# Performance work log

Hardware: AMD Instinct MI355X
Metric: run time of the kernel (lower is better)

Reference implementation:

```python
import jax, jax.numpy as jnp
import numpy as np

NEG_INF = jnp.float32(-1e30)


def setup_inputs() -> dict:
    key = jax.random.key(0)
    k1, k2, k3, k4 = jax.random.split(key, 4)
    B, L1, L2, H = 64, 1024, 1024, 128
    x = jax.random.normal(k1, (B, L1, H), dtype=jnp.float32)
    y = jax.random.normal(k2, (B, L2, H), dtype=jnp.float32)
    y_mask = jax.random.uniform(k3, (B, L2)) < 0.2
    W = jax.random.normal(k4, (H, H), dtype=jnp.float32) * (1.0 / np.sqrt(H))
    b = jnp.zeros((H,), dtype=jnp.float32)
    return {"x": x, "y": y, "y_mask": y_mask, "W": W, "b": b}


def reference(x, y, y_mask, W, b):
    # shared linear + relu projections (torch Linear: x @ W.T + b)
    x_proj = jax.nn.relu(jnp.einsum("bld,hd->blh", x, W) + b)  # [B, L1, H]
    y_proj = jax.nn.relu(jnp.einsum("bld,hd->blh", y, W) + b)  # [B, L2, H]
    # unscaled cross-attention scores
    scores = jnp.einsum("bih,bjh->bij", x_proj, y_proj)  # [B, L1, L2]
    scores = jnp.where(y_mask[:, None, :], NEG_INF, scores)
    alpha = jax.nn.softmax(scores, axis=-1)  # [B, L1, L2]
    # weighted sum over original (unprojected) y
    matched_seq = jnp.einsum("bij,bjh->bih", alpha, y)  # [B, L1, H]
    return matched_seq
```

## Files before the change

kernel.cpp:

```cpp
#include <hip/hip_runtime.h>
#include <hip/hip_bf16.h>


typedef __attribute__((ext_vector_type(8))) short    s8v;
typedef __attribute__((ext_vector_type(8))) _Float16 h8v;
typedef __attribute__((ext_vector_type(4))) _Float16 h4v;
typedef __attribute__((ext_vector_type(4))) float    f4v;

#define BDIM 256

__device__ __forceinline__ f4v mfma_bf16(s8v a, s8v b, f4v c) {
    return __builtin_amdgcn_mfma_f32_16x16x32_bf16(a, b, c, 0, 0, 0);
}
__device__ __forceinline__ f4v mfma_f16(h8v a, h8v b, f4v c) {
    return __builtin_amdgcn_mfma_f32_16x16x32_f16(a, b, c, 0, 0, 0);
}
__device__ __forceinline__ void tsplit(float v, short& hi, short& lo) {
    unsigned b = __builtin_bit_cast(unsigned, v);
    unsigned hb = b & 0xFFFF0000u;
    float res = v - __builtin_bit_cast(float, hb);
    hi = (short)(hb >> 16);
    lo = (short)(__builtin_bit_cast(unsigned, res) >> 16);
}

typedef const __attribute__((address_space(1))) unsigned int gu32;
typedef __attribute__((address_space(3))) unsigned int lu32;
__device__ __forceinline__ void gld_lds16(const void* g, void* l) {
    __builtin_amdgcn_global_load_lds((gu32*)g, (lu32*)l, 16, 0, 0);
}

__global__ __launch_bounds__(1024) void prep_kernel(
    const unsigned int* __restrict__ mraw, unsigned int* __restrict__ orw,
    const float* __restrict__ W, short* __restrict__ Whsw, short* __restrict__ Wlsw)
{
    if (blockIdx.x == 1) {
        for (int idx = threadIdx.x; idx < 16384; idx += 1024) {
            int r = idx >> 7, c = idx & 127;
            short hi, lo; tsplit(W[idx], hi, lo);
            int cs = (((c >> 3) ^ (r & 15)) << 3) | (c & 7);
            Whsw[r * 128 + cs] = hi;
            Wlsw[r * 128 + cs] = lo;
        }
        return;
    }
    __shared__ unsigned int sOrAll, sOrOdd;
    if (threadIdx.x == 0) { sOrAll = 0u; sOrOdd = 0u; }
    __syncthreads();
    unsigned int oa = 0u, oo = 0u;
    for (int i = threadIdx.x; i < 16384; i += 1024) {
        unsigned int v = mraw[i];
        oa |= v;
        if (i & 1) oo |= v;
    }
    atomicOr(&sOrAll, oa);
    atomicOr(&sOrOdd, oo);
    __syncthreads();
    if (threadIdx.x == 0) { orw[0] = sOrAll; orw[1] = sOrOdd; }
}

__global__ __launch_bounds__(BDIM, 4) void proj_kernel(
    const float* __restrict__ X, const float* __restrict__ Y,
    const short* __restrict__ Whsw, const short* __restrict__ Wlsw,
    const float* __restrict__ bias, const unsigned int* __restrict__ orw,
    const unsigned int* __restrict__ mraw, unsigned char* __restrict__ nm,
    _Float16* __restrict__ XPf, _Float16* __restrict__ YPsw,
    _Float16* __restrict__ YTsw)
{
    __shared__ short sW[2][64][128];

    const int gid = blockIdx.x;
    const float* src; int local;
    const bool isY = (gid >= 1024);
    if (!isY) { src = X; local = gid; }
    else      { src = Y; local = gid - 1024; }
    const int row0 = (local >> 1) * 128, h0 = (local & 1) * 64;
    const int t = threadIdx.x, w = t >> 6, lane = t & 63, c = lane & 15, q = lane >> 4;

    {
        const short* g0 = Whsw + h0 * 128;
        const short* g1 = Wlsw + h0 * 128;
        short* l0 = &sW[0][0][0];
        short* l1 = &sW[1][0][0];
        for (int i = 0; i < 4; ++i) {
            int off = (t + i * BDIM) * 8;
            *(s8v*)(l0 + off) = *(const s8v*)(g0 + off);
            *(s8v*)(l1 + off) = *(const s8v*)(g1 + off);
        }
    }

    f4v rawA[2][4], rawB[2][4];
#pragma unroll
    for (int set = 0; set < 2; ++set) {
        const float* xr = src + (size_t)(row0 + w * 32 + set * 16 + c) * 128;
#pragma unroll
        for (int ks = 0; ks < 4; ++ks) {
            rawA[set][ks] = *(const f4v*)&xr[ks * 32 + q * 8];
            rawB[set][ks] = *(const f4v*)&xr[ks * 32 + q * 8 + 4];
        }
    }
    __syncthreads();

    f4v zero = {0.f, 0.f, 0.f, 0.f};
    h4v res[2][4];
#pragma unroll
    for (int set = 0; set < 2; ++set) {
        s8v ah[4], al[4];
#pragma unroll
        for (int ks = 0; ks < 4; ++ks) {
            for (int k = 0; k < 4; ++k) {
                short hh, ll;
                tsplit(rawA[set][ks][k], hh, ll); ah[ks][k] = hh;     al[ks][k] = ll;
                tsplit(rawB[set][ks][k], hh, ll); ah[ks][4 + k] = hh; al[ks][4 + k] = ll;
            }
        }
        f4v acc[4];
        for (int n = 0; n < 4; ++n) acc[n] = zero;
#pragma unroll
        for (int ks = 0; ks < 4; ++ks) {
            s8v bh[4], bl[4];
            for (int nt = 0; nt < 4; ++nt) {
                int cs = (((ks * 4 + q) ^ c) << 3);
                bh[nt] = *(const s8v*)&sW[0][nt * 16 + c][cs];
                bl[nt] = *(const s8v*)&sW[1][nt * 16 + c][cs];
            }
            for (int nt = 0; nt < 4; ++nt) {
                acc[nt] = mfma_bf16(ah[ks], bh[nt], acc[nt]);
                acc[nt] = mfma_bf16(al[ks], bh[nt], acc[nt]);
                acc[nt] = mfma_bf16(ah[ks], bl[nt], acc[nt]);
            }
        }
        for (int nt = 0; nt < 4; ++nt) {
            float bv = bias[h0 + nt * 16 + c];
            for (int r = 0; r < 4; ++r)
                res[set][nt][r] = (_Float16)fmaxf(acc[nt][r] + bv, 0.0f);
        }
    }

    __syncthreads();
    _Float16* sE = (_Float16*)&sW[0][0][0];
#pragma unroll
    for (int set = 0; set < 2; ++set)
        for (int nt = 0; nt < 4; ++nt)
            for (int r = 0; r < 4; ++r) {
                int lr = w * 32 + set * 16 + q * 4 + r;
                int col;
                if (isY) col = (((2 * nt + (c >> 3)) ^ (lr & 7)) << 3) | (c & 7);
                else     col = nt * 16 + c;
                sE[lr * 72 + col] = res[set][nt][r];
            }
    __syncthreads();
    if (!isY) {
        for (int i = 0; i < 4; ++i) {
            int idx = t + i * BDIM;
            int lr = idx >> 3, pos = (idx & 7) * 8;
            *(h8v*)(XPf + (size_t)(row0 + lr) * 128 + h0 + pos) =
                *(const h8v*)(sE + lr * 72 + pos);
        }
    } else {
        for (int i = 0; i < 4; ++i) {
            int idx = t + i * BDIM;
            int lr = idx >> 3, pos = (idx & 7) * 8;
            *(h8v*)(YPsw + (size_t)((row0 + lr) >> 6) * 8192
                    + (size_t)(lr & 63) * 128 + h0 + pos) =
                *(const h8v*)(sE + lr * 72 + pos);
        }
    }

    if (isY && h0 == 0) {
        __syncthreads();
        _Float16* sT = (_Float16*)&sW[0][0][0];
#pragma unroll
        for (int set = 0; set < 2; ++set) {
            int row = w * 32 + set * 16 + c;
            int tile = row >> 6, j6 = row & 63;
            int jlo = j6 & 7, jhb = (j6 >> 3);
#pragma unroll
            for (int ks = 0; ks < 4; ++ks) {
                for (int k = 0; k < 4; ++k) {
                    int h = ks * 32 + q * 8 + k;
                    sT[tile * 8192 + h * 64 + (((jhb ^ (h & 7)) << 3) | jlo)] =
                        (_Float16)rawA[set][ks][k];
                    int h2 = h + 4;
                    sT[tile * 8192 + h2 * 64 + (((jhb ^ (h2 & 7)) << 3) | jlo)] =
                        (_Float16)rawB[set][ks][k];
                }
            }
        }
        __syncthreads();
        _Float16* dst = YTsw + (size_t)(row0 >> 6) * 8192;
        for (int i = 0; i < 8; ++i) {
            int idx = t + i * BDIM;
            *(h8v*)(dst + idx * 8) = *(const h8v*)(sT + idx * 8);
        }
    }

    if (gid < 64) {
        const unsigned orv = orw[0], oro = orw[1];
        int mode;
        if (orv <= 1u)                       mode = (orv == 1u && oro == 0u) ? 3 : 0;
        else if ((orv & 0xFEFEFEFEu) == 0u)  mode = 1;
        else if ((orv & 0x0000FFFFu) == 0u)  mode = 0;
        else                                 mode = 2;
        const unsigned char*  b8  = (const unsigned char*)mraw;
        const unsigned short* b16 = (const unsigned short*)mraw;
        const int base = gid * 1024;
        for (int i = t; i < 1024; i += BDIM) {
            int j = base + i;
            unsigned v;
            if (mode == 0)      v = mraw[j];
            else if (mode == 1) v = b8[j];
            else if (mode == 2) v = b16[j];
            else                v = mraw[2 * j] | mraw[2 * j + 1];
            nm[j] = v ? 1 : 0;
        }
    }
}

__global__ __launch_bounds__(512, 4) void attn_kernel(
    const _Float16* __restrict__ YPsw, const _Float16* __restrict__ YTsw,
    const unsigned char* __restrict__ nmask,
    const _Float16* __restrict__ XPf, float* __restrict__ out)
{
    __shared__ _Float16 sTile[2][16384];
    __shared__ _Float16 sP[128 * 64];

    const int id = blockIdx.x;
    const int xcd = id & 7, rest = id >> 3;
    const int ibase = (rest & 7) * 128;
    const int b = xcd + 8 * (rest >> 3);
    const int t = threadIdx.x, wave = t >> 6, lane = t & 63;
    const int c = lane & 15, q = lane >> 4;
    const int mrow = b * 1024;

    h8v afrag[4];
    {
        const _Float16* xr = XPf + (size_t)(mrow + ibase + wave * 16 + c) * 128;
        for (int ks = 0; ks < 4; ++ks)
            afrag[ks] = *(const h8v*)&xr[ks * 32 + q * 8];
    }

    const char* gYP = (const char*)(YPsw + (size_t)b * 16 * 8192);
    const char* gYT = (const char*)(YTsw + (size_t)b * 16 * 8192);
    const int soff = wave * 1024 + lane * 16;

    {
        char* lp = (char*)&sTile[0][0]    + wave * 1024;
        char* lt = (char*)&sTile[0][8192] + wave * 1024;
        for (int i = 0; i < 2; ++i) {
            gld_lds16(gYP + soff + i * 8192, lp + i * 8192);
            gld_lds16(gYT + soff + i * 8192, lt + i * 8192);
        }
    }

    unsigned mw[4];
    for (int nt = 0; nt < 4; ++nt)
        mw[nt] = *(const unsigned*)(nmask + mrow + nt * 16 + q * 4);

    f4v zero = {0.f, 0.f, 0.f, 0.f};
    float m_s = -INFINITY, l_s = 0.f;
    f4v o[8];
    for (int h = 0; h < 8; ++h) o[h] = zero;

    const int srcbase = (lane & 48) + ((lane >> 4) << 2);
    const int cb = q ^ (c & 7);
    const int prow = (wave * 16 + c) * 64;
    const int pwofs = (q & 1) * 4;

    __syncthreads();

    int cur = 0;
    for (int jt = 0; jt < 16; ++jt) {
        const int jbase = jt * 64;
        const int nx = cur ^ 1;

        if (jt < 15) {
            const char* gp = gYP + (size_t)(jt + 1) * 16384;
            const char* gt = gYT + (size_t)(jt + 1) * 16384;
            char* lp = (char*)&sTile[nx][0]    + wave * 1024;
            char* lt = (char*)&sTile[nx][8192] + wave * 1024;
            for (int i = 0; i < 2; ++i) {
                gld_lds16(gp + soff + i * 8192, lp + i * 8192);
                gld_lds16(gt + soff + i * 8192, lt + i * 8192);
            }
        }

        f4v s[4];
        __builtin_amdgcn_s_setprio(1);
        for (int nt = 0; nt < 4; ++nt) {
            const _Float16* rp = &sTile[cur][0] + (nt * 16 + c) * 128;
            h8v f0 = *(const h8v*)(rp + ((cb ^ 0) << 3));
            h8v f1 = *(const h8v*)(rp + ((cb ^ 4) << 3));
            h8v f2 = *(const h8v*)(rp + ((cb ^ 8) << 3));
            h8v f3 = *(const h8v*)(rp + ((cb ^ 12) << 3));
            f4v acc = zero;
            acc = mfma_f16(f0, afrag[0], acc);
            acc = mfma_f16(f1, afrag[1], acc);
            acc = mfma_f16(f2, afrag[2], acc);
            acc = mfma_f16(f3, afrag[3], acc);
            s[nt] = acc;
        }
        __builtin_amdgcn_s_setprio(0);

        for (int nt = 0; nt < 4; ++nt)
            for (int r = 0; r < 4; ++r)
                if ((mw[nt] >> (r * 8)) & 0xFFu) s[nt][r] = -1e30f;

        float mx = fmaxf(
            fmaxf(fmaxf(fmaxf(s[0][0], s[0][1]), fmaxf(s[0][2], s[0][3])),
                  fmaxf(fmaxf(s[1][0], s[1][1]), fmaxf(s[1][2], s[1][3]))),
            fmaxf(fmaxf(fmaxf(s[2][0], s[2][1]), fmaxf(s[2][2], s[2][3])),
                  fmaxf(fmaxf(s[3][0], s[3][1]), fmaxf(s[3][2], s[3][3]))));
        mx = fmaxf(mx, __shfl_xor(mx, 16, 64));
        mx = fmaxf(mx, __shfl_xor(mx, 32, 64));
        float mnew = fmaxf(m_s, mx);
        float alpha = __expf(m_s - mnew);
        m_s = mnew;

        float rsum = 0.f;
        for (int nt = 0; nt < 4; ++nt) {
            h4v ph4;
            for (int r = 0; r < 4; ++r) {
                float p = ((mw[nt] >> (r * 8)) & 0xFFu) ? 0.f
                          : __expf(s[nt][r] - mnew);
                _Float16 ph = (_Float16)p;
                rsum += (float)ph;
                ph4[r] = ph;
            }
            int ck = (2 * nt + (q >> 1)) ^ (c & 7);
            *(h4v*)&sP[prow + ck * 8 + pwofs] = ph4;
        }
        rsum += __shfl_xor(rsum, 16, 64);
        rsum += __shfl_xor(rsum, 32, 64);
        l_s = l_s * alpha + rsum;

        if (jt < 15) {
            const int jn = jbase + 64;
            for (int nt = 0; nt < 4; ++nt)
                mw[nt] = *(const unsigned*)(nmask + mrow + jn + nt * 16 + q * 4);
        }

        float aD0 = __shfl(alpha, srcbase + 0, 64);
        float aD1 = __shfl(alpha, srcbase + 1, 64);
        float aD2 = __shfl(alpha, srcbase + 2, 64);
        float aD3 = __shfl(alpha, srcbase + 3, 64);
        for (int h = 0; h < 8; ++h) {
            o[h][0] *= aD0; o[h][1] *= aD1; o[h][2] *= aD2; o[h][3] *= aD3;
        }

        __builtin_amdgcn_s_setprio(1);
        for (int k2 = 0; k2 < 2; ++k2) {
            h8v a = *(const h8v*)&sP[prow + (((k2 << 2) + q) ^ (c & 7)) * 8];
            const _Float16* yt = &sTile[cur][8192];
            for (int hb = 0; hb < 8; ++hb) {
                h8v bb = *(const h8v*)(yt + (hb * 16 + c) * 64
                                       + ((((k2 << 2) + q) ^ (c & 7)) << 3));
                o[hb] = mfma_f16(a, bb, o[hb]);
            }
        }
        __builtin_amdgcn_s_setprio(0);

        __syncthreads();
        cur = nx;
    }

    float lD[4];
    lD[0] = __shfl(l_s, srcbase + 0, 64);
    lD[1] = __shfl(l_s, srcbase + 1, 64);
    lD[2] = __shfl(l_s, srcbase + 2, 64);
    lD[3] = __shfl(l_s, srcbase + 3, 64);
    for (int h = 0; h < 8; ++h) {
        for (int r = 0; r < 4; ++r) {
            float v = o[h][r] / lD[r];
            out[(size_t)(mrow + ibase + wave * 16 + q * 4 + r) * 128 + h * 16 + c] = v;
        }
    }
}

extern "C" void kernel_launch(void* const* d_in, const int* in_sizes, int n_in,
                              void* d_out, int out_size, void* d_ws, size_t ws_size,
                              hipStream_t stream) {
    const float* x    = (const float*)d_in[0];
    const float* y    = (const float*)d_in[1];
    const unsigned int* mraw = (const unsigned int*)d_in[2];
    const float* W    = (const float*)d_in[3];
    const float* bias = (const float*)d_in[4];
    float* out = (float*)d_out;

    unsigned char* nmask = (unsigned char*)d_ws;
    short* Whsw = (short*)((char*)d_ws + 65536);
    short* Wlsw = Whsw + 16384;
    unsigned int* orw = (unsigned int*)((char*)d_ws + 131072);
    _Float16* XPf = (_Float16*)((char*)d_ws + 135168);
    _Float16* YPsw = XPf + (size_t)64 * 1024 * 128;
    _Float16* YTsw = YPsw + (size_t)64 * 1024 * 128;

    prep_kernel<<<2, 1024, 0, stream>>>(mraw, orw, W, Whsw, Wlsw);
    proj_kernel<<<2048, BDIM, 0, stream>>>(x, y, Whsw, Wlsw, bias, orw,
                                           mraw, nmask, XPf, YPsw, YTsw);
    attn_kernel<<<512, 512, 0, stream>>>(YPsw, YTsw, nmask, XPf, out);
}
```

Before: 199.7 us.

## Fuse prep into projection kernel and compute both output halves per block

Removes the separate prep kernel launch. The weight bf16 hi/lo split and swizzle now happen inside each projection block, and the mask OR-reduction is recomputed per block for the first 64 blocks. Each block now computes all 128 output columns in two passes over the same loaded input rows instead of two blocks each loading the rows for 64 columns, halving input reads and grid size. In exchange, every block redundantly converts the full W from global fp32, occupancy drops, and the Y transpose is written by every Y block.

```diff
diff --git a/kernel.cpp b/kernel.cpp
--- a/kernel.cpp
+++ b/kernel.cpp
@@ -29,63 +29,34 @@
     __builtin_amdgcn_global_load_lds((gu32*)g, (lu32*)l, 16, 0, 0);
 }
 
-__global__ __launch_bounds__(1024) void prep_kernel(
-    const unsigned int* __restrict__ mraw, unsigned int* __restrict__ orw,
-    const float* __restrict__ W, short* __restrict__ Whsw, short* __restrict__ Wlsw)
-{
-    if (blockIdx.x == 1) {
-        for (int idx = threadIdx.x; idx < 16384; idx += 1024) {
-            int r = idx >> 7, c = idx & 127;
-            short hi, lo; tsplit(W[idx], hi, lo);
-            int cs = (((c >> 3) ^ (r & 15)) << 3) | (c & 7);
-            Whsw[r * 128 + cs] = hi;
-            Wlsw[r * 128 + cs] = lo;
-        }
-        return;
-    }
-    __shared__ unsigned int sOrAll, sOrOdd;
-    if (threadIdx.x == 0) { sOrAll = 0u; sOrOdd = 0u; }
-    __syncthreads();
-    unsigned int oa = 0u, oo = 0u;
-    for (int i = threadIdx.x; i < 16384; i += 1024) {
-        unsigned int v = mraw[i];
-        oa |= v;
-        if (i & 1) oo |= v;
-    }
-    atomicOr(&sOrAll, oa);
-    atomicOr(&sOrOdd, oo);
-    __syncthreads();
-    if (threadIdx.x == 0) { orw[0] = sOrAll; orw[1] = sOrOdd; }
-}
-
-__global__ __launch_bounds__(BDIM, 4) void proj_kernel(
+__global__ __launch_bounds__(BDIM, 3) void proj_kernel(
     const float* __restrict__ X, const float* __restrict__ Y,
-    const short* __restrict__ Whsw, const short* __restrict__ Wlsw,
-    const float* __restrict__ bias, const unsigned int* __restrict__ orw,
+    const float* __restrict__ W, const float* __restrict__ bias,
     const unsigned int* __restrict__ mraw, unsigned char* __restrict__ nm,
     _Float16* __restrict__ XPf, _Float16* __restrict__ YPsw,
     _Float16* __restrict__ YTsw)
 {
     __shared__ short sW[2][64][128];
+    __shared__ _Float16 sE[128 * 72];
+    __shared__ unsigned sOr[2];
 
     const int gid = blockIdx.x;
-    const float* src; int local;
-    const bool isY = (gid >= 1024);
-    if (!isY) { src = X; local = gid; }
-    else      { src = Y; local = gid - 1024; }
-    const int row0 = (local >> 1) * 128, h0 = (local & 1) * 64;
+    const bool isY = (gid >= 512);
+    const int local = isY ? gid - 512 : gid;
+    const float* src = isY ? Y : X;
+    const int row0 = local * 128;
     const int t = threadIdx.x, w = t >> 6, lane = t & 63, c = lane & 15, q = lane >> 4;
 
-    {
-        const short* g0 = Whsw + h0 * 128;
-        const short* g1 = Wlsw + h0 * 128;
-        short* l0 = &sW[0][0][0];
-        short* l1 = &sW[1][0][0];
-        for (int i = 0; i < 4; ++i) {
-            int off = (t + i * BDIM) * 8;
-            *(s8v*)(l0 + off) = *(const s8v*)(g0 + off);
-            *(s8v*)(l1 + off) = *(const s8v*)(g1 + off);
-        }
+    if (t == 0) { sOr[0] = 0u; sOr[1] = 0u; }
+
+#pragma unroll 4
+    for (int i = 0; i < 32; ++i) {
+        int idx = t + i * BDIM;
+        int rr = idx >> 7, c2 = idx & 127;
+        short hi, lo; tsplit(W[rr * 128 + c2], hi, lo);
+        int cs = (((c2 >> 3) ^ (rr & 15)) << 3) | (c2 & 7);
+        sW[0][rr][cs] = hi;
+        sW[1][rr][cs] = lo;
     }
 
     f4v rawA[2][4], rawB[2][4];
@@ -102,17 +73,17 @@
 
     f4v zero = {0.f, 0.f, 0.f, 0.f};
     h4v res[2][4];
+
 #pragma unroll
     for (int set = 0; set < 2; ++set) {
         s8v ah[4], al[4];
 #pragma unroll
-        for (int ks = 0; ks < 4; ++ks) {
+        for (int ks = 0; ks < 4; ++ks)
             for (int k = 0; k < 4; ++k) {
                 short hh, ll;
                 tsplit(rawA[set][ks][k], hh, ll); ah[ks][k] = hh;     al[ks][k] = ll;
                 tsplit(rawB[set][ks][k], hh, ll); ah[ks][4 + k] = hh; al[ks][4 + k] = ll;
             }
-        }
         f4v acc[4];
         for (int n = 0; n < 4; ++n) acc[n] = zero;
 #pragma unroll
@@ -130,14 +101,22 @@
             }
         }
         for (int nt = 0; nt < 4; ++nt) {
-            float bv = bias[h0 + nt * 16 + c];
+            float bv = bias[nt * 16 + c];
             for (int r = 0; r < 4; ++r)
                 res[set][nt][r] = (_Float16)fmaxf(acc[nt][r] + bv, 0.0f);
         }
     }
-
-    __syncthreads();
-    _Float16* sE = (_Float16*)&sW[0][0][0];
+    __syncthreads();
+
+#pragma unroll 4
+    for (int i = 0; i < 32; ++i) {
+        int idx = t + i * BDIM;
+        int rr = idx >> 7, c2 = idx & 127;
+        short hi, lo; tsplit(W[(64 + rr) * 128 + c2], hi, lo);
+        int cs = (((c2 >> 3) ^ (rr & 15)) << 3) | (c2 & 7);
+        sW[0][rr][cs] = hi;
+        sW[1][rr][cs] = lo;
+    }
 #pragma unroll
     for (int set = 0; set < 2; ++set)
         for (int nt = 0; nt < 4; ++nt)
@@ -149,11 +128,12 @@
                 sE[lr * 72 + col] = res[set][nt][r];
             }
     __syncthreads();
+
     if (!isY) {
         for (int i = 0; i < 4; ++i) {
             int idx = t + i * BDIM;
             int lr = idx >> 3, pos = (idx & 7) * 8;
-            *(h8v*)(XPf + (size_t)(row0 + lr) * 128 + h0 + pos) =
+            *(h8v*)(XPf + (size_t)(row0 + lr) * 128 + pos) =
                 *(const h8v*)(sE + lr * 72 + pos);
         }
     } else {
@@ -161,13 +141,56 @@
             int idx = t + i * BDIM;
             int lr = idx >> 3, pos = (idx & 7) * 8;
             *(h8v*)(YPsw + (size_t)((row0 + lr) >> 6) * 8192
-                    + (size_t)(lr & 63) * 128 + h0 + pos) =
+                    + (size_t)(lr & 63) * 128 + pos) =
                 *(const h8v*)(sE + lr * 72 + pos);
         }
     }
 
-    if (isY && h0 == 0) {
-        __syncthreads();
+#pragma unroll
+    for (int set = 0; set < 2; ++set) {
+        s8v ah[4], al[4];
+#pragma unroll
+        for (int ks = 0; ks < 4; ++ks)
+            for (int k = 0; k < 4; ++k) {
+                short hh, ll;
+                tsplit(rawA[set][ks][k], hh, ll); ah[ks][k] = hh;     al[ks][k] = ll;
+                tsplit(rawB[set][ks][k], hh, ll); ah[ks][4 + k] = hh; al[ks][4 + k] = ll;
+            }
+        f4v acc[4];
+        for (int n = 0; n < 4; ++n) acc[n] = zero;
+#pragma unroll
+        for (int ks = 0; ks < 4; ++ks) {
+            s8v bh[4], bl[4];
+            for (int nt = 0; nt < 4; ++nt) {
+                int cs = (((ks * 4 + q) ^ c) << 3);
+                bh[nt] = *(const s8v*)&sW[0][nt * 16 + c][cs];
+                bl[nt] = *(const s8v*)&sW[1][nt * 16 + c][cs];
+            }
+            for (int nt = 0; nt < 4; ++nt) {
+                acc[nt] = mfma_bf16(ah[ks], bh[nt], acc[nt]);
+                acc[nt] = mfma_bf16(al[ks], bh[nt], acc[nt]);
+                acc[nt] = mfma_bf16(ah[ks], bl[nt], acc[nt]);
+            }
+        }
+        for (int nt = 0; nt < 4; ++nt) {
+            float bv = bias[64 + nt * 16 + c];
+            for (int r = 0; r < 4; ++r)
+                res[set][nt][r] = (_Float16)fmaxf(acc[nt][r] + bv, 0.0f);
+        }
+    }
+    __syncthreads();
+
+#pragma unroll
+    for (int set = 0; set < 2; ++set)
+        for (int nt = 0; nt < 4; ++nt)
+            for (int r = 0; r < 4; ++r) {
+                int lr = w * 32 + set * 16 + q * 4 + r;
+                int col;
+                if (isY) col = (((2 * nt + (c >> 3)) ^ (lr & 7)) << 3) | (c & 7);
+                else     col = nt * 16 + c;
+                sE[lr * 72 + col] = res[set][nt][r];
+            }
+    if (isY) {
         _Float16* sT = (_Float16*)&sW[0][0][0];
 #pragma unroll
         for (int set = 0; set < 2; ++set) {
@@ -175,7 +198,7 @@
             int tile = row >> 6, j6 = row & 63;
             int jlo = j6 & 7, jhb = (j6 >> 3);
 #pragma unroll
-            for (int ks = 0; ks < 4; ++ks) {
+            for (int ks = 0; ks < 4; ++ks)
                 for (int k = 0; k < 4; ++k) {
                     int h = ks * 32 + q * 8 + k;
                     sT[tile * 8192 + h * 64 + (((jhb ^ (h & 7)) << 3) | jlo)] =
@@ -184,10 +207,27 @@
                     sT[tile * 8192 + h2 * 64 + (((jhb ^ (h2 & 7)) << 3) | jlo)] =
                         (_Float16)rawB[set][ks][k];
                 }
-            }
-        }
-        __syncthreads();
-        _Float16* dst = YTsw + (size_t)(row0 >> 6) * 8192;
+        }
+    }
+    __syncthreads();
+
+    if (!isY) {
+        for (int i = 0; i < 4; ++i) {
+            int idx = t + i * BDIM;
+            int lr = idx >> 3, pos = (idx & 7) * 8;
+            *(h8v*)(XPf + (size_t)(row0 + lr) * 128 + 64 + pos) =
+                *(const h8v*)(sE + lr * 72 + pos);
+        }
+    } else {
+        for (int i = 0; i < 4; ++i) {
+            int idx = t + i * BDIM;
+            int lr = idx >> 3, pos = (idx & 7) * 8;
+            *(h8v*)(YPsw + (size_t)((row0 + lr) >> 6) * 8192
+                    + (size_t)(lr & 63) * 128 + 64 + pos) =
+                *(const h8v*)(sE + lr * 72 + pos);
+        }
+        const _Float16* sT = (const _Float16*)&sW[0][0][0];
+        _Float16* dst = YTsw + (size_t)(local * 2) * 8192;
         for (int i = 0; i < 8; ++i) {
             int idx = t + i * BDIM;
             *(h8v*)(dst + idx * 8) = *(const h8v*)(sT + idx * 8);
@@ -195,7 +235,16 @@
     }
 
     if (gid < 64) {
-        const unsigned orv = orw[0], oro = orw[1];
+        unsigned oa = 0u, oo = 0u;
+        for (int i = t; i < 16384; i += BDIM) {
+            unsigned v = mraw[i];
+            oa |= v;
+            if (i & 1) oo |= v;
+        }
+        atomicOr(&sOr[0], oa);
+        atomicOr(&sOr[1], oo);
+        __syncthreads();
+        const unsigned orv = sOr[0], oro = sOr[1];
         int mode;
         if (orv <= 1u)                       mode = (orv == 1u && oro == 0u) ? 3 : 0;
         else if ((orv & 0xFEFEFEFEu) == 0u)  mode = 1;
@@ -387,15 +436,11 @@
     float* out = (float*)d_out;
 
     unsigned char* nmask = (unsigned char*)d_ws;
-    short* Whsw = (short*)((char*)d_ws + 65536);
-    short* Wlsw = Whsw + 16384;
-    unsigned int* orw = (unsigned int*)((char*)d_ws + 131072);
-    _Float16* XPf = (_Float16*)((char*)d_ws + 135168);
+    _Float16* XPf = (_Float16*)((char*)d_ws + 65536);
     _Float16* YPsw = XPf + (size_t)64 * 1024 * 128;
     _Float16* YTsw = YPsw + (size_t)64 * 1024 * 128;
 
-    prep_kernel<<<2, 1024, 0, stream>>>(mraw, orw, W, Whsw, Wlsw);
-    proj_kernel<<<2048, BDIM, 0, stream>>>(x, y, Whsw, Wlsw, bias, orw,
-                                           mraw, nmask, XPf, YPsw, YTsw);
+    proj_kernel<<<1024, BDIM, 0, stream>>>(x, y, W, bias, mraw, nmask,
+                                           XPf, YPsw, YTsw);
     attn_kernel<<<512, 512, 0, stream>>>(YPsw, YTsw, nmask, XPf, out);
 }
```

After: 232.4 us. +16.4%, slower.

## Fuse X projection into attention kernel instead of materializing XPf

Applied to the files above, without the earlier changes.

The X-side linear+ReLU projection moves out of proj_kernel and into attn_kernel's prologue. Each attention block now loads its own fp32 X rows, runs the bf16 split-precision MFMA projection against W staged in shared memory, and builds the A fragments directly. This drops the XPf fp16 write and re-read through global memory and halves the projection grid. In exchange the attention kernel does extra W loads, MFMAs and barriers before its main loop.

```diff
diff --git a/kernel.cpp b/kernel.cpp
--- a/kernel.cpp
+++ b/kernel.cpp
@@ -59,21 +59,16 @@
 }
 
 __global__ __launch_bounds__(BDIM, 4) void proj_kernel(
-    const float* __restrict__ X, const float* __restrict__ Y,
+    const float* __restrict__ Y,
     const short* __restrict__ Whsw, const short* __restrict__ Wlsw,
     const float* __restrict__ bias, const unsigned int* __restrict__ orw,
     const unsigned int* __restrict__ mraw, unsigned char* __restrict__ nm,
-    _Float16* __restrict__ XPf, _Float16* __restrict__ YPsw,
-    _Float16* __restrict__ YTsw)
+    _Float16* __restrict__ YPsw, _Float16* __restrict__ YTsw)
 {
     __shared__ short sW[2][64][128];
 
     const int gid = blockIdx.x;
-    const float* src; int local;
-    const bool isY = (gid >= 1024);
-    if (!isY) { src = X; local = gid; }
-    else      { src = Y; local = gid - 1024; }
-    const int row0 = (local >> 1) * 128, h0 = (local & 1) * 64;
+    const int row0 = (gid >> 1) * 128, h0 = (gid & 1) * 64;
     const int t = threadIdx.x, w = t >> 6, lane = t & 63, c = lane & 15, q = lane >> 4;
 
     {
@@ -91,7 +86,7 @@
     f4v rawA[2][4], rawB[2][4];
 #pragma unroll
     for (int set = 0; set < 2; ++set) {
-        const float* xr = src + (size_t)(row0 + w * 32 + set * 16 + c) * 128;
+        const float* xr = Y + (size_t)(row0 + w * 32 + set * 16 + c) * 128;
 #pragma unroll
         for (int ks = 0; ks < 4; ++ks) {
             rawA[set][ks] = *(const f4v*)&xr[ks * 32 + q * 8];
@@ -106,13 +101,12 @@
     for (int set = 0; set < 2; ++set) {
         s8v ah[4], al[4];
 #pragma unroll
-        for (int ks = 0; ks < 4; ++ks) {
+        for (int ks = 0; ks < 4; ++ks)
             for (int k = 0; k < 4; ++k) {
                 short hh, ll;
                 tsplit(rawA[set][ks][k], hh, ll); ah[ks][k] = hh;     al[ks][k] = ll;
                 tsplit(rawB[set][ks][k], hh, ll); ah[ks][4 + k] = hh; al[ks][4 + k] = ll;
             }
-        }
         f4v acc[4];
         for (int n = 0; n < 4; ++n) acc[n] = zero;
 #pragma unroll
@@ -143,30 +137,19 @@
         for (int nt = 0; nt < 4; ++nt)
             for (int r = 0; r < 4; ++r) {
                 int lr = w * 32 + set * 16 + q * 4 + r;
-                int col;
-                if (isY) col = (((2 * nt + (c >> 3)) ^ (lr & 7)) << 3) | (c & 7);
-                else     col = nt * 16 + c;
+                int col = (((2 * nt + (c >> 3)) ^ (lr & 7)) << 3) | (c & 7);
                 sE[lr * 72 + col] = res[set][nt][r];
             }
     __syncthreads();
-    if (!isY) {
-        for (int i = 0; i < 4; ++i) {
-            int idx = t + i * BDIM;
-            int lr = idx >> 3, pos = (idx & 7) * 8;
-            *(h8v*)(XPf + (size_t)(row0 + lr) * 128 + h0 + pos) =
-                *(const h8v*)(sE + lr * 72 + pos);
-        }
-    } else {
-        for (int i = 0; i < 4; ++i) {
-            int idx = t + i * BDIM;
-            int lr = idx >> 3, pos = (idx & 7) * 8;
-            *(h8v*)(YPsw + (size_t)((row0 + lr) >> 6) * 8192
-                    + (size_t)(lr & 63) * 128 + h0 + pos) =
-                *(const h8v*)(sE + lr * 72 + pos);
-        }
-    }
-
-    if (isY && h0 == 0) {
+    for (int i = 0; i < 4; ++i) {
+        int idx = t + i * BDIM;
+        int lr = idx >> 3, pos = (idx & 7) * 8;
+        *(h8v*)(YPsw + (size_t)((row0 + lr) >> 6) * 8192
+                + (size_t)(lr & 63) * 128 + h0 + pos) =
+            *(const h8v*)(sE + lr * 72 + pos);
+    }
+
+    if (h0 == 0) {
         __syncthreads();
         _Float16* sT = (_Float16*)&sW[0][0][0];
 #pragma unroll
@@ -175,7 +158,7 @@
             int tile = row >> 6, j6 = row & 63;
             int jlo = j6 & 7, jhb = (j6 >> 3);
 #pragma unroll
-            for (int ks = 0; ks < 4; ++ks) {
+            for (int ks = 0; ks < 4; ++ks)
                 for (int k = 0; k < 4; ++k) {
                     int h = ks * 32 + q * 8 + k;
                     sT[tile * 8192 + h * 64 + (((jhb ^ (h & 7)) << 3) | jlo)] =
@@ -184,7 +167,6 @@
                     sT[tile * 8192 + h2 * 64 + (((jhb ^ (h2 & 7)) << 3) | jlo)] =
                         (_Float16)rawB[set][ks][k];
                 }
-            }
         }
         __syncthreads();
         _Float16* dst = YTsw + (size_t)(row0 >> 6) * 8192;
@@ -217,9 +199,11 @@
 }
 
 __global__ __launch_bounds__(512, 4) void attn_kernel(
+    const float* __restrict__ X,
+    const short* __restrict__ Whsw, const short* __restrict__ Wlsw,
+    const float* __restrict__ bias,
     const _Float16* __restrict__ YPsw, const _Float16* __restrict__ YTsw,
-    const unsigned char* __restrict__ nmask,
-    const _Float16* __restrict__ XPf, float* __restrict__ out)
+    const unsigned char* __restrict__ nmask, float* __restrict__ out)
 {
     __shared__ _Float16 sTile[2][16384];
     __shared__ _Float16 sP[128 * 64];
@@ -232,11 +216,71 @@
     const int c = lane & 15, q = lane >> 4;
     const int mrow = b * 1024;
 
+    f4v zero = {0.f, 0.f, 0.f, 0.f};
+
     h8v afrag[4];
     {
-        const _Float16* xr = XPf + (size_t)(mrow + ibase + wave * 16 + c) * 128;
+        f4v rawA[4], rawB[4];
+        const float* xr = X + (size_t)(mrow + ibase + wave * 16 + c) * 128;
+#pragma unroll
+        for (int ks = 0; ks < 4; ++ks) {
+            rawA[ks] = *(const f4v*)&xr[ks * 32 + q * 8];
+            rawB[ks] = *(const f4v*)&xr[ks * 32 + q * 8 + 4];
+        }
+        s8v ah[4], al[4];
+#pragma unroll
         for (int ks = 0; ks < 4; ++ks)
-            afrag[ks] = *(const h8v*)&xr[ks * 32 + q * 8];
+            for (int k = 0; k < 4; ++k) {
+                short hh, ll;
+                tsplit(rawA[ks][k], hh, ll); ah[ks][k] = hh;     al[ks][k] = ll;
+                tsplit(rawB[ks][k], hh, ll); ah[ks][4 + k] = hh; al[ks][4 + k] = ll;
+            }
+
+        short* sWp = (short*)&sTile[0][0];
+        _Float16* sE = sP;
+
+#pragma unroll
+        for (int half = 0; half < 2; ++half) {
+            const int h0 = half * 64;
+            {
+                const short* g0 = Whsw + h0 * 128;
+                const short* g1 = Wlsw + h0 * 128;
+                for (int i = 0; i < 2; ++i) {
+                    int off = (t + i * 512) * 8;
+                    *(s8v*)(sWp + off)        = *(const s8v*)(g0 + off);
+                    *(s8v*)(sWp + 8192 + off) = *(const s8v*)(g1 + off);
+                }
+            }
+            __syncthreads();
+
+            f4v acc[4];
+            for (int n = 0; n < 4; ++n) acc[n] = zero;
+#pragma unroll
+            for (int ks = 0; ks < 4; ++ks) {
+                s8v bh[4], bl[4];
+                for (int nt = 0; nt < 4; ++nt) {
+                    int cs = (((ks * 4 + q) ^ c) << 3);
+                    bh[nt] = *(const s8v*)&sWp[(nt * 16 + c) * 128 + cs];
+                    bl[nt] = *(const s8v*)&sWp[8192 + (nt * 16 + c) * 128 + cs];
+                }
+                for (int nt = 0; nt < 4; ++nt) {
+                    acc[nt] = mfma_bf16(ah[ks], bh[nt], acc[nt]);
+                    acc[nt] = mfma_bf16(al[ks], bh[nt], acc[nt]);
+                    acc[nt] = mfma_bf16(ah[ks], bl[nt], acc[nt]);
+                }
+            }
+            __syncthreads();
+            for (int nt = 0; nt < 4; ++nt) {
+                float bv = bias[h0 + nt * 16 + c];
+                for (int r = 0; r < 4; ++r)
+                    sE[(wave * 16 + q * 4 + r) * 64 + nt * 16 + c] =
+                        (_Float16)fmaxf(acc[nt][r] + bv, 0.0f);
+            }
+            __syncthreads();
+            afrag[half * 2]     = *(const h8v*)&sE[(wave * 16 + c) * 64 + q * 8];
+            afrag[half * 2 + 1] = *(const h8v*)&sE[(wave * 16 + c) * 64 + 32 + q * 8];
+        }
+        __syncthreads();
     }
 
     const char* gYP = (const char*)(YPsw + (size_t)b * 16 * 8192);
@@ -256,7 +300,6 @@
     for (int nt = 0; nt < 4; ++nt)
         mw[nt] = *(const unsigned*)(nmask + mrow + nt * 16 + q * 4);
 
-    f4v zero = {0.f, 0.f, 0.f, 0.f};
     float m_s = -INFINITY, l_s = 0.f;
     f4v o[8];
     for (int h = 0; h < 8; ++h) o[h] = zero;
@@ -390,12 +433,12 @@
     short* Whsw = (short*)((char*)d_ws + 65536);
     short* Wlsw = Whsw + 16384;
     unsigned int* orw = (unsigned int*)((char*)d_ws + 131072);
-    _Float16* XPf = (_Float16*)((char*)d_ws + 135168);
-    _Float16* YPsw = XPf + (size_t)64 * 1024 * 128;
+    _Float16* YPsw = (_Float16*)((char*)d_ws + 135168);
     _Float16* YTsw = YPsw + (size_t)64 * 1024 * 128;
 
     prep_kernel<<<2, 1024, 0, stream>>>(mraw, orw, W, Whsw, Wlsw);
-    proj_kernel<<<2048, BDIM, 0, stream>>>(x, y, Whsw, Wlsw, bias, orw,
-                                           mraw, nmask, XPf, YPsw, YTsw);
-    attn_kernel<<<512, 512, 0, stream>>>(YPsw, YTsw, nmask, XPf, out);
-}
+    proj_kernel<<<1024, BDIM, 0, stream>>>(y, Whsw, Wlsw, bias, orw,
+                                           mraw, nmask, YPsw, YTsw);
+    attn_kernel<<<512, 512, 0, stream>>>(x, Whsw, Wlsw, bias,
+                                         YPsw, YTsw, nmask, out);
+}
```

Result: faster. 195.4 us (-2.2%).
